# Kernel tuning notes

Hardware: AMD Instinct MI355X
Metric: run time of the kernel (lower is better)

The kernel has to match this reference:

```python
import jax, jax.numpy as jnp
import numpy as np

VOC_SIZE = 32768
DIM = 512
NUM_TOPK = 64
BATCH = 4096


def setup_inputs() -> dict:
    key = jax.random.key(0)
    ks = jax.random.split(key, 8)
    lim = 1.0 / np.sqrt(DIM)  # kaiming_uniform(a=sqrt(5)) on [V, d] -> U(-1/sqrt(d), 1/sqrt(d))
    x = jax.random.normal(ks[0], (BATCH, DIM), dtype=jnp.float32)
    codebook = jax.random.uniform(ks[1], (VOC_SIZE, DIM), dtype=jnp.float32, minval=-lim, maxval=lim)
    Wq = jax.random.uniform(ks[2], (DIM, DIM), dtype=jnp.float32, minval=-lim, maxval=lim)
    bq = jax.random.uniform(ks[3], (DIM,), dtype=jnp.float32, minval=-lim, maxval=lim)
    Wk = jax.random.uniform(ks[4], (DIM, DIM), dtype=jnp.float32, minval=-lim, maxval=lim)
    bk = jax.random.uniform(ks[5], (DIM,), dtype=jnp.float32, minval=-lim, maxval=lim)
    Wv = jax.random.uniform(ks[6], (DIM, DIM), dtype=jnp.float32, minval=-lim, maxval=lim)
    bv = jax.random.uniform(ks[7], (DIM,), dtype=jnp.float32, minval=-lim, maxval=lim)
    return {"x": x, "codebook": codebook, "Wq": Wq, "bq": bq,
            "Wk": Wk, "bk": bk, "Wv": Wv, "bv": bv}


def reference(x, codebook, Wq, bq, Wk, bk, Wv, bv):
    # projections (torch Linear with weight stored pre-transposed as [in, out])
    q = x @ Wq + bq              # [B, d]
    k = codebook @ Wk + bk       # [V, d]
    v = codebook @ Wv + bv       # [V, d]

    dots = jnp.einsum('bd,kd->bk', q, k)              # [B, V]
    top, _ = jax.lax.top_k(dots, NUM_TOPK)            # [B, num_topk]
    thresh = top[..., -1:]                            # k-th largest value per row
    mask_value = -jnp.finfo(dots.dtype).max
    dots = jnp.where(dots < thresh, mask_value, dots)
    attn = jax.nn.softmax(dots, axis=-1)              # [B, V]
    out = jnp.einsum('bk,kd->bd', attn, v)            # [B, d]
    return out
```

## Files before the change

kernel.cpp:

```cpp
#include <hip/hip_runtime.h>
#include <cstdint>

#define VOC   32768
#define DIM   512
#define TOPK  64
#define BATCH 4096

#define KSIG     2.45f
#define EPS_SEL  0.012f
#define CAND_CAP 512
#define RES_CAP  256
#define FCAP     1024

typedef unsigned short u16;
typedef __attribute__((ext_vector_type(8))) short bf16x8;
typedef __attribute__((ext_vector_type(4))) float f32x4;

__device__ __forceinline__ u16 f2bf(float f) {
    unsigned u = __float_as_uint(f);
    unsigned r = (u + 0x7FFFu + ((u >> 16) & 1u)) >> 16;
    return (u16)r;
}
__device__ __forceinline__ float bf2f(u16 h) {
    return __uint_as_float(((unsigned)h) << 16);
}
__device__ __forceinline__ unsigned enc16(u16 h) {
    return (h & 0x8000u) ? (unsigned)((u16)~h) : (unsigned)(h | 0x8000u);
}
__device__ __forceinline__ float dec16(unsigned s16) {
    u16 h = (s16 & 0x8000u) ? (u16)(s16 ^ 0x8000u) : (u16)(~s16);
    return bf2f(h);
}

__device__ __forceinline__ void async16(const void* g, void* l) {
    __builtin_amdgcn_global_load_lds(
        (const __attribute__((address_space(1))) void*)g,
        (__attribute__((address_space(3))) void*)l, 16, 0, 0);
}

template <bool BT, bool F64ACC>
__global__ __launch_bounds__(256)
void gemm64(const float* __restrict__ A, const float* __restrict__ B,
            const float* __restrict__ bias, float* __restrict__ C,
            int M, int N, int K)
{
    const int KS = 16;
    __shared__ float As[KS][68];
    __shared__ float Bs[KS][64];

    const int tid = threadIdx.x;
    const int m0 = blockIdx.y * 64;
    const int n0 = blockIdx.x * 64;
    const int ty = tid >> 4;
    const int tx = tid & 15;

    float acc[4][4];
    double acc64[4][4];
#pragma unroll
    for (int i = 0; i < 4; i++)
#pragma unroll
        for (int j = 0; j < 4; j++) { acc[i][j] = 0.f; if (F64ACC) acc64[i][j] = 0.0; }

    for (int kt = 0; kt < K; kt += KS) {
        {
            int row = tid >> 2, kq = tid & 3;
            const float4 av = *(const float4*)(A + (size_t)(m0 + row) * K + kt + kq * 4);
            As[kq * 4 + 0][row] = av.x;
            As[kq * 4 + 1][row] = av.y;
            As[kq * 4 + 2][row] = av.z;
            As[kq * 4 + 3][row] = av.w;
        }
        if (!BT) {
            int krow = tid >> 4, nq = tid & 15;
            *(float4*)&Bs[krow][nq * 4] =
                *(const float4*)(B + (size_t)(kt + krow) * N + n0 + nq * 4);
        } else {
            int nrow = tid >> 2, kq = tid & 3;
            const float4 bv = *(const float4*)(B + (size_t)(n0 + nrow) * K + kt + kq * 4);
            Bs[kq * 4 + 0][nrow] = bv.x;
            Bs[kq * 4 + 1][nrow] = bv.y;
            Bs[kq * 4 + 2][nrow] = bv.z;
            Bs[kq * 4 + 3][nrow] = bv.w;
        }
        __syncthreads();

#pragma unroll
        for (int kk = 0; kk < KS; kk++) {
            float4 a = *(const float4*)&As[kk][ty * 4];
            float4 b = *(const float4*)&Bs[kk][tx * 4];
            float av[4] = {a.x, a.y, a.z, a.w};
            float bv[4] = {b.x, b.y, b.z, b.w};
#pragma unroll
            for (int i = 0; i < 4; i++)
#pragma unroll
                for (int j = 0; j < 4; j++)
                    acc[i][j] += av[i] * bv[j];
        }
        __syncthreads();
        if (F64ACC) {
#pragma unroll
            for (int i = 0; i < 4; i++)
#pragma unroll
                for (int j = 0; j < 4; j++) { acc64[i][j] += (double)acc[i][j]; acc[i][j] = 0.f; }
        }
    }

    float4 bb = make_float4(0.f, 0.f, 0.f, 0.f);
    if (bias) bb = *(const float4*)(bias + n0 + tx * 4);
#pragma unroll
    for (int i = 0; i < 4; i++) {
        float4 o;
        o.x = (F64ACC ? (float)acc64[i][0] : acc[i][0]) + bb.x;
        o.y = (F64ACC ? (float)acc64[i][1] : acc[i][1]) + bb.y;
        o.z = (F64ACC ? (float)acc64[i][2] : acc[i][2]) + bb.z;
        o.w = (F64ACC ? (float)acc64[i][3] : acc[i][3]) + bb.w;
        *(float4*)(C + (size_t)(m0 + ty * 4 + i) * N + n0 + tx * 4) = o;
    }
}

__global__ void bias_fold(const float* __restrict__ bq, const float* __restrict__ Wk,
                          float* __restrict__ bqk)
{
    int j = blockIdx.x * 256 + threadIdx.x;
    if (j >= DIM) return;
    double s = 0.0;
    const float* wr = Wk + (size_t)j * DIM;
    for (int d = 0; d < DIM; d++) s += (double)bq[d] * (double)wr[d];
    bqk[j] = (float)s;
}

__global__ void zero_ws(unsigned* __restrict__ p, int n)
{
    int i = blockIdx.x * 256 + threadIdx.x;
    if (i < n) p[i] = 0u;
}

__global__ __launch_bounds__(256)
void cbar_accum(const float* __restrict__ cb, float* __restrict__ cbarsum)
{
    const int tid = threadIdx.x;
    const int r0 = blockIdx.x * 128;
    float s0 = 0.f, s1 = 0.f;
    for (int r = 0; r < 128; r++) {
        const float* rp = cb + (size_t)(r0 + r) * DIM;
        s0 += rp[tid];
        s1 += rp[tid + 256];
    }
    atomicAdd(&cbarsum[tid], s0);
    atomicAdd(&cbarsum[tid + 256], s1);
}

__global__ __launch_bounds__(256)
void rowstats(const float* __restrict__ q2, const float* __restrict__ cbarsum,
              float* __restrict__ trow, float* __restrict__ sigrow)
{
    const int tid = threadIdx.x, lane = tid & 63, wave = tid >> 6;
    const int row = blockIdx.x * 4 + wave;
    const float* qp = q2 + (size_t)row * DIM + lane * 8;
    float4 a0 = *(const float4*)qp, a1 = *(const float4*)(qp + 4);
    const float* cp = cbarsum + lane * 8;
    float4 c0 = *(const float4*)cp, c1 = *(const float4*)(cp + 4);
    float mu = a0.x*c0.x + a0.y*c0.y + a0.z*c0.z + a0.w*c0.w
             + a1.x*c1.x + a1.y*c1.y + a1.z*c1.z + a1.w*c1.w;
    float nr = a0.x*a0.x + a0.y*a0.y + a0.z*a0.z + a0.w*a0.w
             + a1.x*a1.x + a1.y*a1.y + a1.z*a1.z + a1.w*a1.w;
#pragma unroll
    for (int off = 32; off > 0; off >>= 1) {
        mu += __shfl_down(mu, off);
        nr += __shfl_down(nr, off);
    }
    if (lane == 0) {
        mu *= (1.f / VOC);
        float sig = sqrtf(nr * (1.f / 1536.f));
        trow[row] = mu + KSIG * sig;
        sigrow[row] = sig;
    }
}

__global__ __launch_bounds__(256)
void pack_rows(const float* __restrict__ src, u16* __restrict__ hi,
               u16* __restrict__ lo, int R, int log2R)
{
    int idx = blockIdx.x * 256 + threadIdx.x;
    int c8  = idx >> log2R;
    int row = idx & (R - 1);
    const float* sp = src + (size_t)row * DIM + c8 * 8;
    float xv[8];
    *(float4*)&xv[0] = *(const float4*)sp;
    *(float4*)&xv[4] = *(const float4*)(sp + 4);
    int ks = c8 >> 2, ch = c8 & 3;
    size_t ob = ((size_t)(ks * 4 + ch) * R + row) * 8;
    u16 h[8], l[8];
#pragma unroll
    for (int j = 0; j < 8; j++) {
        h[j] = f2bf(xv[j]);
        l[j] = f2bf(xv[j] - bf2f(h[j]));
    }
    *(uint4*)(hi + ob) = *(const uint4*)h;
    if (lo) *(uint4*)(lo + ob) = *(const uint4*)l;
}

__global__ __launch_bounds__(256)
void pack_bT(const float* __restrict__ W, u16* __restrict__ hi, u16* __restrict__ lo)
{
    int idx = blockIdx.x * 256 + threadIdx.x;
    int n  = idx & (DIM - 1);
    int c8 = idx >> 9;
    int ks = c8 >> 2, ch = c8 & 3;
    size_t ob = ((size_t)(ks * 4 + ch) * DIM + n) * 8;
    u16 h[8], l[8];
#pragma unroll
    for (int j = 0; j < 8; j++) {
        float x = W[(size_t)(c8 * 8 + j) * DIM + n];
        h[j] = f2bf(x);
        l[j] = f2bf(x - bf2f(h[j]));
    }
    *(uint4*)(hi + ob) = *(const uint4*)h;
    *(uint4*)(lo + ob) = *(const uint4*)l;
}

__global__ __launch_bounds__(256, 4)
void mfma_dots(const u16* __restrict__ Ah, const u16* __restrict__ Bh,
               const float* __restrict__ trow, unsigned* __restrict__ candBuf,
               unsigned* __restrict__ counters)
{
    __shared__ u16 lds[2 * 8192];

    const int tid  = threadIdx.x;
    const int lane = tid & 63;
    const int wave = tid >> 6;
    const int wm = wave >> 1, wn = wave & 1;
    const int lr = lane & 15;
    const int q  = lane >> 4;

    const int L   = blockIdx.x;
    const int xcd = L & 7;
    const int j   = L >> 3;
    const int m0  = (xcd * 4 + (j & 3)) * 128;
    const int n0  = (j >> 2) * 128;

    const int a  = wave >> 1;
    const u16* src = a ? Bh : Ah;
    const int rb   = a ? n0 : m0;
    const size_t R = a ? (size_t)VOC : (size_t)BATCH;
    const int i0   = (wave & 1) * 4;

    const size_t gstep = (size_t)4 * R * 8;
    const u16* gp0 = src + ((size_t)(((i0 + 0) >> 1)) * R + rb + ((i0 + 0) & 1) * 64 + lane) * 8;
    const u16* gp1 = src + ((size_t)(((i0 + 1) >> 1)) * R + rb + ((i0 + 1) & 1) * 64 + lane) * 8;
    const u16* gp2 = src + ((size_t)(((i0 + 2) >> 1)) * R + rb + ((i0 + 2) & 1) * 64 + lane) * 8;
    const u16* gp3 = src + ((size_t)(((i0 + 3) >> 1)) * R + rb + ((i0 + 3) & 1) * 64 + lane) * 8;
    const int loff0 = a * 4096 + (i0 + 0) * 512 + lane * 8;
    const int loff1 = a * 4096 + (i0 + 1) * 512 + lane * 8;
    const int loff2 = a * 4096 + (i0 + 2) * 512 + lane * 8;
    const int loff3 = a * 4096 + (i0 + 3) * 512 + lane * 8;

#define ISSUE(b)                                                              \
    {                                                                         \
        async16(gp0, &lds[(b) * 8192 + loff0]); gp0 += gstep;                 \
        async16(gp1, &lds[(b) * 8192 + loff1]); gp1 += gstep;                 \
        async16(gp2, &lds[(b) * 8192 + loff2]); gp2 += gstep;                 \
        async16(gp3, &lds[(b) * 8192 + loff3]); gp3 += gstep;                 \
    }

    f32x4 acc[4][4] = {};

    ISSUE(0)

    for (int s = 0; s < 16; s++) {
        __builtin_amdgcn_s_waitcnt(0x0F70);
        __builtin_amdgcn_s_barrier();
        if (s < 15) ISSUE((s + 1) & 1)
        const u16* base = &lds[(s & 1) * 8192];

        bf16x8 ah[4];
#pragma unroll
        for (int mt = 0; mt < 4; mt++)
            ah[mt] = *(const bf16x8*)&base[q * 1024 + (wm * 64 + mt * 16 + lr) * 8];
        __builtin_amdgcn_s_setprio(1);
#pragma unroll
        for (int nt = 0; nt < 4; nt++) {
            bf16x8 bh = *(const bf16x8*)&base[4096 + q * 1024 + (wn * 64 + nt * 16 + lr) * 8];
#pragma unroll
            for (int mt = 0; mt < 4; mt++)
                acc[mt][nt] = __builtin_amdgcn_mfma_f32_16x16x32_bf16(ah[mt], bh, acc[mt][nt], 0, 0, 0);
        }
        __builtin_amdgcn_s_setprio(0);
    }
#undef ISSUE

#pragma unroll
    for (int mt = 0; mt < 4; mt++) {
#pragma unroll
        for (int r = 0; r < 4; r++) {
            int rowg = m0 + wm * 64 + mt * 16 + q * 4 + r;
            float tr = trow[rowg];
#pragma unroll
            for (int nt = 0; nt < 4; nt++) {
                float val = acc[mt][nt][r];
                if (val >= tr) {
                    unsigned slot = atomicAdd(&counters[rowg], 1u);
                    if (slot < CAND_CAP) {
                        unsigned s16 = enc16(f2bf(val));
                        candBuf[(size_t)rowg * CAND_CAP + slot] =
                            (s16 << 16) | (unsigned)(n0 + wn * 64 + nt * 16 + lr);
                    }
                }
            }
        }
    }
}

__global__ __launch_bounds__(256, 2)
void mfma_out(const u16* __restrict__ Ah, const u16* __restrict__ Al,
              const u16* __restrict__ Bh, const u16* __restrict__ Bl,
              const float* __restrict__ bias, float* __restrict__ Cout, int Ma)
{
    __shared__ u16 lds[2 * 16384];

    const int tid  = threadIdx.x;
    const int lane = tid & 63;
    const int wave = tid >> 6;
    const int wm = wave >> 1, wn = wave & 1;
    const int m0 = blockIdx.y * 128, n0 = blockIdx.x * 128;
    const int lr = lane & 15;
    const int q  = lane >> 4;

    f32x4 acc[4][4] = {};
    const u16* garr[4] = {Ah, Bh, Al, Bl};
    const int a = wave;
    const u16* src = garr[a];
    const bool isA = (a == 0 || a == 2);
    const int rb = isA ? m0 : n0;
    const size_t R = isA ? (size_t)Ma : (size_t)DIM;

#define VISSUE(ks, b)                                                         \
    {                                                                         \
        _Pragma("unroll")                                                     \
        for (int i_ = 0; i_ < 8; i_++) {                                      \
            const u16* gp_ = src + ((size_t)((ks) * 4 + (i_ >> 1)) * R + rb   \
                                    + (i_ & 1) * 64 + lane) * 8;              \
            async16(gp_, &lds[(b) * 16384 + a * 4096 + i_ * 512 + lane * 8]); \
        }                                                                     \
    }

    VISSUE(0, 0)

    for (int ks = 0; ks < 16; ks++) {
        __syncthreads();
        if (ks < 15) VISSUE(ks + 1, (ks + 1) & 1)
        const u16* base = &lds[(ks & 1) * 16384];

        bf16x8 ah[4], al[4];
#pragma unroll
        for (int mt = 0; mt < 4; mt++) {
            int row = wm * 64 + mt * 16 + lr;
            ah[mt] = *(const bf16x8*)&base[0 * 4096 + q * 1024 + row * 8];
            al[mt] = *(const bf16x8*)&base[2 * 4096 + q * 1024 + row * 8];
        }
#pragma unroll
        for (int nt = 0; nt < 4; nt++) {
            int col = wn * 64 + nt * 16 + lr;
            bf16x8 bh = *(const bf16x8*)&base[1 * 4096 + q * 1024 + col * 8];
            bf16x8 bl = *(const bf16x8*)&base[3 * 4096 + q * 1024 + col * 8];
#pragma unroll
            for (int mt = 0; mt < 4; mt++) {
                acc[mt][nt] = __builtin_amdgcn_mfma_f32_16x16x32_bf16(ah[mt], bh, acc[mt][nt], 0, 0, 0);
                acc[mt][nt] = __builtin_amdgcn_mfma_f32_16x16x32_bf16(ah[mt], bl, acc[mt][nt], 0, 0, 0);
                acc[mt][nt] = __builtin_amdgcn_mfma_f32_16x16x32_bf16(al[mt], bh, acc[mt][nt], 0, 0, 0);
            }
        }
    }
#undef VISSUE

#pragma unroll
    for (int mt = 0; mt < 4; mt++)
#pragma unroll
        for (int nt = 0; nt < 4; nt++) {
            int col = n0 + wn * 64 + nt * 16 + lr;
            float bb = bias[col];
#pragma unroll
            for (int r = 0; r < 4; r++) {
                int rowg = m0 + wm * 64 + mt * 16 + q * 4 + r;
                Cout[(size_t)rowg * DIM + col] = acc[mt][nt][r] + bb;
            }
        }
}

__global__ __launch_bounds__(256)
void select6(const unsigned* __restrict__ candBuf, const unsigned* __restrict__ counters,
             const float* __restrict__ trow, const float* __restrict__ q2,
             const float* __restrict__ codebook, float* __restrict__ y,
             unsigned* __restrict__ flags)
{
    __shared__ unsigned recs[CAND_CAP];
    __shared__ unsigned list[RES_CAP];
    __shared__ unsigned hist[256];
    __shared__ unsigned long long keys[RES_CAP];
    __shared__ float q2s[DIM];
    __shared__ float wArr[RES_CAP];
    __shared__ float redf[256];
    __shared__ unsigned redu[256];
    __shared__ unsigned s_R;
    __shared__ unsigned s_b1, s_rem, s_thr;

    const int tid  = threadIdx.x;
    const int lane = tid & 63;
    const int wave = tid >> 6;
    const int row  = blockIdx.x;

    const unsigned cnt = counters[row];
    if (cnt < TOPK || cnt > CAND_CAP) {
        if (tid == 0) flags[row] = 1u;
        return;
    }
    for (int i = tid; i < DIM; i += 256) q2s[i] = q2[(size_t)row * DIM + i];
    for (int i = tid; i < CAND_CAP; i += 256)
        recs[i] = (i < (int)cnt) ? candBuf[(size_t)row * CAND_CAP + i] : 0u;
    if (tid == 0) s_R = 0;
    hist[tid] = 0;
    __syncthreads();

#pragma unroll
    for (int e = 0; e < 2; e++) {
        int i = tid + e * 256;
        if (i < (int)cnt) atomicAdd(&hist[recs[i] >> 24], 1u);
    }
    __syncthreads();
    if (tid == 0) {
        unsigned c = 0; int b = 255;
        for (; b > 0; b--) {
            unsigned h = hist[b];
            if (c + h >= TOPK) break;
            c += h;
        }
        s_b1 = (unsigned)b; s_rem = TOPK - c;
    }
    __syncthreads();
    const unsigned b1 = s_b1, rem = s_rem;
    hist[tid] = 0;
    __syncthreads();

#pragma unroll
    for (int e = 0; e < 2; e++) {
        int i = tid + e * 256;
        if (i < (int)cnt && (recs[i] >> 24) == b1)
            atomicAdd(&hist[(recs[i] >> 16) & 0xFFu], 1u);
    }
    __syncthreads();
    if (tid == 0) {
        unsigned c = 0; int b = 255;
        for (; b > 0; b--) {
            unsigned h = hist[b];
            if (c + h >= rem) break;
            c += h;
        }
        s_thr = (b1 << 8) | (unsigned)b;
    }
    __syncthreads();

    const float a64  = dec16(s_thr);
    const float band = a64 - 2.f * EPS_SEL;
    if (trow[row] > band) {
        if (tid == 0) flags[row] = 1u;
        return;
    }

#pragma unroll
    for (int e = 0; e < 2; e++) {
        int i = tid + e * 256;
        if (i < (int)cnt && dec16(recs[i] >> 16) >= band) {
            unsigned p = atomicAdd(&s_R, 1u);
            if (p < RES_CAP) list[p] = recs[i];
        }
    }
    __syncthreads();
    const int R = (int)s_R;
    if (R > RES_CAP) {
        if (tid == 0) flags[row] = 1u;
        return;
    }

    for (int c = wave; c < R; c += 4) {
        unsigned idx = list[c] & 0xFFFFu;
        const float* cb = codebook + (size_t)idx * DIM + lane * 8;
        float4 c0 = *(const float4*)cb, c1 = *(const float4*)(cb + 4);
        const float* qp = &q2s[lane * 8];
        float4 a0 = *(const float4*)qp, a1 = *(const float4*)(qp + 4);
        double s = (double)a0.x * c0.x + (double)a0.y * c0.y
                 + (double)a0.z * c0.z + (double)a0.w * c0.w
                 + (double)a1.x * c1.x + (double)a1.y * c1.y
                 + (double)a1.z * c1.z + (double)a1.w * c1.w;
#pragma unroll
        for (int off = 32; off > 0; off >>= 1) s += __shfl_down(s, off);
        if (lane == 0) {
            float val = (float)s;
            unsigned b = __float_as_uint(val);
            unsigned sk = (b & 0x80000000u) ? ~b : (b | 0x80000000u);
            keys[c] = ((unsigned long long)(~sk) << 32) | idx;
        }
    }
    if (tid >= R && tid < RES_CAP) keys[tid] = ~0ULL;
    __syncthreads();

    for (int k = 2; k <= RES_CAP; k <<= 1) {
        for (int j = k >> 1; j > 0; j >>= 1) {
            int ixj = tid ^ j;
            if (ixj > tid) {
                unsigned long long a = keys[tid], b2 = keys[ixj];
                if (((tid & k) == 0) ? (a > b2) : (a < b2)) { keys[tid] = b2; keys[ixj] = a; }
            }
            __syncthreads();
        }
    }

    const unsigned threshInv = (unsigned)(keys[TOPK - 1] >> 32);
    unsigned sk0 = ~(unsigned)(keys[0] >> 32);
    const float vmax = __uint_as_float((sk0 & 0x80000000u) ? (sk0 & 0x7FFFFFFFu) : ~sk0);

    unsigned hi = (unsigned)(keys[tid] >> 32);
    bool sel = (hi <= threshInv);
    unsigned sk = ~hi;
    float val = __uint_as_float((sk & 0x80000000u) ? (sk & 0x7FFFFFFFu) : ~sk);
    float w = sel ? expf(val - vmax) : 0.f;
    wArr[tid] = w;
    redf[tid] = w;
    redu[tid] = sel ? 1u : 0u;
    __syncthreads();
    for (int s = 128; s > 0; s >>= 1) {
        if (tid < s) { redf[tid] += redf[tid + s]; redu[tid] += redu[tid + s]; }
        __syncthreads();
    }
    const float invZ = 1.0f / redf[0];
    const int selCount = (int)redu[0];

    for (int d = tid; d < DIM; d += 256) {
        float acc = 0.f;
        for (int i = 0; i < selCount; i++) {
            unsigned idx = (unsigned)(keys[i] & 0xFFFFFFFFu);
            acc += wArr[i] * codebook[(size_t)idx * DIM + d];
        }
        y[(size_t)row * DIM + d] = acc * invZ;
    }
}

__global__ __launch_bounds__(256)
void fallback_row(const unsigned* __restrict__ flags, const float* __restrict__ q2,
                  const float* __restrict__ codebook, const float* __restrict__ trow,
                  const float* __restrict__ sigrow, float* __restrict__ y)
{
    const int row = blockIdx.x;
    if (!flags[row]) return;

    __shared__ float q2s[DIM];
    __shared__ unsigned long long keys[FCAP];
    __shared__ float wArr[FCAP];
    __shared__ float redf[256];
    __shared__ unsigned redu[256];
    __shared__ unsigned s_cnt;

    const int tid = threadIdx.x;
    for (int i = tid; i < DIM; i += 256) q2s[i] = q2[(size_t)row * DIM + i];
    const float sig = sigrow[row];
    float tf = trow[row] - 0.35f * sig;
    unsigned cnt = 0;

    for (int it = 0; it < 16; it++) {
        if (tid == 0) s_cnt = 0;
        __syncthreads();
        for (int i = tid; i < VOC; i += 256) {
            const float* cb = codebook + (size_t)i * DIM;
            double s = 0.0;
            for (int d = 0; d < DIM; d += 4) {
                float4 c4 = *(const float4*)(cb + d);
                s += (double)q2s[d + 0] * (double)c4.x + (double)q2s[d + 1] * (double)c4.y
                   + (double)q2s[d + 2] * (double)c4.z + (double)q2s[d + 3] * (double)c4.w;
            }
            float vv = (float)s;
            if (vv >= tf) {
                unsigned p = atomicAdd(&s_cnt, 1u);
                if (p < FCAP) {
                    unsigned b = __float_as_uint(vv);
                    unsigned sk = (b & 0x80000000u) ? ~b : (b | 0x80000000u);
                    keys[p] = ((unsigned long long)(~sk) << 32) | (unsigned)i;
                }
            }
        }
        __syncthreads();
        cnt = s_cnt;
        if (cnt > FCAP) { tf += 0.15f * sig; continue; }
        if (cnt < TOPK) { tf -= 0.35f * sig; continue; }
        break;
    }
    if (cnt > FCAP) cnt = FCAP;
    for (int i = tid; i < FCAP; i += 256)
        if (i >= (int)cnt) keys[i] = ~0ULL;
    __syncthreads();

    for (int k = 2; k <= FCAP; k <<= 1) {
        for (int j = k >> 1; j > 0; j >>= 1) {
#pragma unroll
            for (int e = 0; e < 4; e++) {
                int i = tid + e * 256;
                int ixj = i ^ j;
                if (ixj > i) {
                    unsigned long long a = keys[i], b = keys[ixj];
                    if (((i & k) == 0) ? (a > b) : (a < b)) { keys[i] = b; keys[ixj] = a; }
                }
            }
            __syncthreads();
        }
    }

    const unsigned threshInv = (unsigned)(keys[TOPK - 1] >> 32);
    unsigned sk0 = ~(unsigned)(keys[0] >> 32);
    const float vmax = __uint_as_float((sk0 & 0x80000000u) ? (sk0 & 0x7FFFFFFFu) : ~sk0);

    float lsum = 0.f; unsigned lcnt = 0;
    for (int i = tid; i < FCAP; i += 256) {
        unsigned hi = (unsigned)(keys[i] >> 32);
        bool sel = (hi <= threshInv);
        unsigned sk = ~hi;
        float vv = __uint_as_float((sk & 0x80000000u) ? (sk & 0x7FFFFFFFu) : ~sk);
        float w = sel ? expf(vv - vmax) : 0.f;
        wArr[i] = w;
        lsum += w; lcnt += sel ? 1u : 0u;
    }
    redf[tid] = lsum; redu[tid] = lcnt;
    __syncthreads();
    for (int s = 128; s > 0; s >>= 1) {
        if (tid < s) { redf[tid] += redf[tid + s]; redu[tid] += redu[tid + s]; }
        __syncthreads();
    }
    const float invZ = 1.f / redf[0];
    const int selCount = (int)redu[0];

    for (int d = tid; d < DIM; d += 256) {
        float acc = 0.f;
        for (int i = 0; i < selCount; i++) {
            unsigned idx = (unsigned)(keys[i] & 0xFFFFFFFFu);
            acc += wArr[i] * codebook[(size_t)idx * DIM + d];
        }
        y[(size_t)row * DIM + d] = acc * invZ;
    }
}

extern "C" void kernel_launch(void* const* d_in, const int* in_sizes, int n_in,
                              void* d_out, int out_size, void* d_ws, size_t ws_size,
                              hipStream_t stream)
{
    const float* x        = (const float*)d_in[0];
    const float* codebook = (const float*)d_in[1];
    const float* Wq       = (const float*)d_in[2];
    const float* bq       = (const float*)d_in[3];
    const float* Wk       = (const float*)d_in[4];
    const float* Wv       = (const float*)d_in[6];
    const float* bv       = (const float*)d_in[7];
    float* out = (float*)d_out;

    float* q2   = (float*)d_ws;
    float* Wqk  = q2   + (size_t)BATCH * DIM;
    float* bqk  = Wqk  + (size_t)DIM * DIM;
    float* y    = bqk  + 1024;
    float* trow = y    + (size_t)BATCH * DIM;
    float* sigr = trow + BATCH;
    unsigned* counters = (unsigned*)(sigr + BATCH);
    unsigned* flags    = counters + BATCH;
    float* cbarsum     = (float*)(flags + BATCH);
    unsigned* candBuf  = (unsigned*)(cbarsum + 512);
    u16* q2h = (u16*)(candBuf + (size_t)BATCH * CAND_CAP);
    u16* cbh = q2h + (size_t)BATCH * DIM;
    u16* yh  = cbh + (size_t)VOC * DIM;
    u16* yl  = yh  + (size_t)BATCH * DIM;
    u16* wvh = yl  + (size_t)BATCH * DIM;
    u16* wvl = wvh + (size_t)DIM * DIM;

    u16* xh   = yh;
    u16* xl   = yl;
    u16* wqkh = (u16*)candBuf;
    u16* wqkl = wqkh + (size_t)DIM * DIM;

    dim3 blk(256);

    gemm64<true, true><<<dim3(DIM / 64, DIM / 64), blk, 0, stream>>>(
        Wq, Wk, nullptr, Wqk, DIM, DIM, DIM);
    bias_fold<<<dim3(2), blk, 0, stream>>>(bq, Wk, bqk);

    pack_bT<<<dim3(DIM * 64 / 256), blk, 0, stream>>>(Wqk, wqkh, wqkl);
    pack_rows<<<dim3(BATCH * 64 / 256), blk, 0, stream>>>(x, xh, xl, BATCH, 12);
    mfma_out<<<dim3(DIM / 128, BATCH / 128), blk, 0, stream>>>(
        xh, xl, wqkh, wqkl, bqk, q2, BATCH);

    zero_ws<<<dim3(34), blk, 0, stream>>>(counters, BATCH * 2 + 512);

    cbar_accum<<<dim3(VOC / 128), blk, 0, stream>>>(codebook, cbarsum);
    rowstats<<<dim3(BATCH / 4), blk, 0, stream>>>(q2, cbarsum, trow, sigr);

    pack_rows<<<dim3(BATCH * 64 / 256), blk, 0, stream>>>(q2, q2h, nullptr, BATCH, 12);
    pack_rows<<<dim3(VOC * 64 / 256), blk, 0, stream>>>(codebook, cbh, nullptr, VOC, 15);
    pack_bT<<<dim3(DIM * 64 / 256), blk, 0, stream>>>(Wv, wvh, wvl);

    mfma_dots<<<dim3(8192), blk, 0, stream>>>(q2h, cbh, trow, candBuf, counters);

    select6<<<dim3(BATCH), blk, 0, stream>>>(
        candBuf, counters, trow, q2, codebook, y, flags);
    fallback_row<<<dim3(BATCH), blk, 0, stream>>>(
        flags, q2, codebook, trow, sigr, y);

    pack_rows<<<dim3(BATCH * 64 / 256), blk, 0, stream>>>(y, yh, yl, BATCH, 12);
    mfma_out<<<dim3(DIM / 128, BATCH / 128), blk, 0, stream>>>(
        yh, yl, wvh, wvl, bv, out, BATCH);
}
```

Before: 678.9 us.

## Load B fragments directly to registers in mfma_dots and parallelize bias_fold

After: 689.7 us. About the same (+1.6%).

```diff
diff --git a/kernel.cpp b/kernel.cpp
--- a/kernel.cpp
+++ b/kernel.cpp
@@ -118,15 +118,20 @@
     }
 }
 
-__global__ void bias_fold(const float* __restrict__ bq, const float* __restrict__ Wk,
-                          float* __restrict__ bqk)
-{
-    int j = blockIdx.x * 256 + threadIdx.x;
-    if (j >= DIM) return;
+__global__ __launch_bounds__(256)
+void bias_fold(const float* __restrict__ bq, const float* __restrict__ Wk,
+               float* __restrict__ bqk)
+{
+    const int lane = threadIdx.x & 63, wave = threadIdx.x >> 6;
+    const int j = blockIdx.x * 4 + wave;
+    const float* wr = Wk + (size_t)j * DIM + lane * 8;
+    const float* bp = bq + lane * 8;
     double s = 0.0;
-    const float* wr = Wk + (size_t)j * DIM;
-    for (int d = 0; d < DIM; d++) s += (double)bq[d] * (double)wr[d];
-    bqk[j] = (float)s;
+#pragma unroll
+    for (int t = 0; t < 8; t++) s += (double)bp[t] * (double)wr[t];
+#pragma unroll
+    for (int off = 32; off > 0; off >>= 1) s += __shfl_down(s, off);
+    if (lane == 0) bqk[j] = (float)s;
 }
 
 __global__ void zero_ws(unsigned* __restrict__ p, int n)
@@ -224,7 +229,7 @@
                const float* __restrict__ trow, unsigned* __restrict__ candBuf,
                unsigned* __restrict__ counters)
 {
-    __shared__ u16 lds[2 * 8192];
+    __shared__ u16 lds[4 * 4096];
 
     const int tid  = threadIdx.x;
     const int lane = tid & 63;
@@ -239,55 +244,53 @@
     const int m0  = (xcd * 4 + (j & 3)) * 128;
     const int n0  = (j >> 2) * 128;
 
-    const int a  = wave >> 1;
-    const u16* src = a ? Bh : Ah;
-    const int rb   = a ? n0 : m0;
-    const size_t R = a ? (size_t)VOC : (size_t)BATCH;
-    const int i0   = (wave & 1) * 4;
-
-    const size_t gstep = (size_t)4 * R * 8;
-    const u16* gp0 = src + ((size_t)(((i0 + 0) >> 1)) * R + rb + ((i0 + 0) & 1) * 64 + lane) * 8;
-    const u16* gp1 = src + ((size_t)(((i0 + 1) >> 1)) * R + rb + ((i0 + 1) & 1) * 64 + lane) * 8;
-    const u16* gp2 = src + ((size_t)(((i0 + 2) >> 1)) * R + rb + ((i0 + 2) & 1) * 64 + lane) * 8;
-    const u16* gp3 = src + ((size_t)(((i0 + 3) >> 1)) * R + rb + ((i0 + 3) & 1) * 64 + lane) * 8;
-    const int loff0 = a * 4096 + (i0 + 0) * 512 + lane * 8;
-    const int loff1 = a * 4096 + (i0 + 1) * 512 + lane * 8;
-    const int loff2 = a * 4096 + (i0 + 2) * 512 + lane * 8;
-    const int loff3 = a * 4096 + (i0 + 3) * 512 + lane * 8;
-
-#define ISSUE(b)                                                              \
-    {                                                                         \
-        async16(gp0, &lds[(b) * 8192 + loff0]); gp0 += gstep;                 \
-        async16(gp1, &lds[(b) * 8192 + loff1]); gp1 += gstep;                 \
-        async16(gp2, &lds[(b) * 8192 + loff2]); gp2 += gstep;                 \
-        async16(gp3, &lds[(b) * 8192 + loff3]); gp3 += gstep;                 \
-    }
+    u16* wlds = &lds[wave * 4096];
+
+#define AISSUE(ks, st)                                                         \
+    { _Pragma("unroll")                                                        \
+      for (int ch_ = 0; ch_ < 4; ch_++) {                                      \
+          const u16* gp_ = Ah + ((size_t)((ks) * 4 + ch_) * BATCH              \
+                                 + m0 + wm * 64 + lane) * 8;                   \
+          async16(gp_, &wlds[(st) * 2048 + ch_ * 512 + lane * 8]);             \
+      } }
+
+#define BPTR(nt, ks) ((const bf16x8*)(Bh + ((size_t)((ks) * 4 + q) * VOC       \
+                                            + n0 + wn * 64 + (nt) * 16 + lr) * 8))
 
     f32x4 acc[4][4] = {};
-
-    ISSUE(0)
-
+    bf16x8 bb[2][4];
+
+    AISSUE(0, 0)
+#pragma unroll
+    for (int nt = 0; nt < 4; nt++) bb[0][nt] = *BPTR(nt, 0);
+
+#pragma unroll
     for (int s = 0; s < 16; s++) {
+        const int st = s & 1;
         __builtin_amdgcn_s_waitcnt(0x0F70);
-        __builtin_amdgcn_s_barrier();
-        if (s < 15) ISSUE((s + 1) & 1)
-        const u16* base = &lds[(s & 1) * 8192];
 
         bf16x8 ah[4];
 #pragma unroll
         for (int mt = 0; mt < 4; mt++)
-            ah[mt] = *(const bf16x8*)&base[q * 1024 + (wm * 64 + mt * 16 + lr) * 8];
+            ah[mt] = *(const bf16x8*)&wlds[st * 2048 + q * 512 + (mt * 16 + lr) * 8];
+
+        __builtin_amdgcn_sched_barrier(0);
+        __builtin_amdgcn_s_waitcnt(0xC47F);
+        if (s < 15) AISSUE(s + 1, st ^ 1)
+
         __builtin_amdgcn_s_setprio(1);
 #pragma unroll
         for (int nt = 0; nt < 4; nt++) {
-            bf16x8 bh = *(const bf16x8*)&base[4096 + q * 1024 + (wn * 64 + nt * 16 + lr) * 8];
+            if (s < 15) bb[st ^ 1][nt] = *BPTR(nt, s + 1);
 #pragma unroll
             for (int mt = 0; mt < 4; mt++)
-                acc[mt][nt] = __builtin_amdgcn_mfma_f32_16x16x32_bf16(ah[mt], bh, acc[mt][nt], 0, 0, 0);
+                acc[mt][nt] = __builtin_amdgcn_mfma_f32_16x16x32_bf16(
+                    ah[mt], bb[st][nt], acc[mt][nt], 0, 0, 0);
         }
         __builtin_amdgcn_s_setprio(0);
     }
-#undef ISSUE
+#undef AISSUE
+#undef BPTR
 
 #pragma unroll
     for (int mt = 0; mt < 4; mt++) {
@@ -684,7 +687,7 @@
 
     gemm64<true, true><<<dim3(DIM / 64, DIM / 64), blk, 0, stream>>>(
         Wq, Wk, nullptr, Wqk, DIM, DIM, DIM);
-    bias_fold<<<dim3(2), blk, 0, stream>>>(bq, Wk, bqk);
+    bias_fold<<<dim3(DIM / 4), blk, 0, stream>>>(bq, Wk, bqk);
 
     pack_bT<<<dim3(DIM * 64 / 256), blk, 0, stream>>>(Wqk, wqkh, wqkl);
     pack_rows<<<dim3(BATCH * 64 / 256), blk, 0, stream>>>(x, xh, xl, BATCH, 12);
```

## Fuse prep kernels into two launches and restructure dots loop prefetch

Applied to the files above, without the earlier changes.

Result: faster. 643.0 us (-5.3%).

```diff
diff --git a/kernel.cpp b/kernel.cpp
--- a/kernel.cpp
+++ b/kernel.cpp
@@ -118,70 +118,17 @@
     }
 }
 
-__global__ void bias_fold(const float* __restrict__ bq, const float* __restrict__ Wk,
-                          float* __restrict__ bqk)
-{
-    int j = blockIdx.x * 256 + threadIdx.x;
-    if (j >= DIM) return;
-    double s = 0.0;
-    const float* wr = Wk + (size_t)j * DIM;
-    for (int d = 0; d < DIM; d++) s += (double)bq[d] * (double)wr[d];
-    bqk[j] = (float)s;
-}
-
 __global__ void zero_ws(unsigned* __restrict__ p, int n)
 {
     int i = blockIdx.x * 256 + threadIdx.x;
     if (i < n) p[i] = 0u;
 }
 
-__global__ __launch_bounds__(256)
-void cbar_accum(const float* __restrict__ cb, float* __restrict__ cbarsum)
-{
-    const int tid = threadIdx.x;
-    const int r0 = blockIdx.x * 128;
-    float s0 = 0.f, s1 = 0.f;
-    for (int r = 0; r < 128; r++) {
-        const float* rp = cb + (size_t)(r0 + r) * DIM;
-        s0 += rp[tid];
-        s1 += rp[tid + 256];
-    }
-    atomicAdd(&cbarsum[tid], s0);
-    atomicAdd(&cbarsum[tid + 256], s1);
-}
-
-__global__ __launch_bounds__(256)
-void rowstats(const float* __restrict__ q2, const float* __restrict__ cbarsum,
-              float* __restrict__ trow, float* __restrict__ sigrow)
-{
-    const int tid = threadIdx.x, lane = tid & 63, wave = tid >> 6;
-    const int row = blockIdx.x * 4 + wave;
-    const float* qp = q2 + (size_t)row * DIM + lane * 8;
-    float4 a0 = *(const float4*)qp, a1 = *(const float4*)(qp + 4);
-    const float* cp = cbarsum + lane * 8;
-    float4 c0 = *(const float4*)cp, c1 = *(const float4*)(cp + 4);
-    float mu = a0.x*c0.x + a0.y*c0.y + a0.z*c0.z + a0.w*c0.w
-             + a1.x*c1.x + a1.y*c1.y + a1.z*c1.z + a1.w*c1.w;
-    float nr = a0.x*a0.x + a0.y*a0.y + a0.z*a0.z + a0.w*a0.w
-             + a1.x*a1.x + a1.y*a1.y + a1.z*a1.z + a1.w*a1.w;
-#pragma unroll
-    for (int off = 32; off > 0; off >>= 1) {
-        mu += __shfl_down(mu, off);
-        nr += __shfl_down(nr, off);
-    }
-    if (lane == 0) {
-        mu *= (1.f / VOC);
-        float sig = sqrtf(nr * (1.f / 1536.f));
-        trow[row] = mu + KSIG * sig;
-        sigrow[row] = sig;
-    }
-}
-
-__global__ __launch_bounds__(256)
-void pack_rows(const float* __restrict__ src, u16* __restrict__ hi,
-               u16* __restrict__ lo, int R, int log2R)
-{
-    int idx = blockIdx.x * 256 + threadIdx.x;
+__device__ __forceinline__ void pack_rows_dev(int bid, int tid,
+        const float* __restrict__ src, u16* __restrict__ hi,
+        u16* __restrict__ lo, int R, int log2R)
+{
+    int idx = bid * 256 + tid;
     int c8  = idx >> log2R;
     int row = idx & (R - 1);
     const float* sp = src + (size_t)row * DIM + c8 * 8;
@@ -200,10 +147,10 @@
     if (lo) *(uint4*)(lo + ob) = *(const uint4*)l;
 }
 
-__global__ __launch_bounds__(256)
-void pack_bT(const float* __restrict__ W, u16* __restrict__ hi, u16* __restrict__ lo)
-{
-    int idx = blockIdx.x * 256 + threadIdx.x;
+__device__ __forceinline__ void pack_bT_dev(int bid, int tid,
+        const float* __restrict__ W, u16* __restrict__ hi, u16* __restrict__ lo)
+{
+    int idx = bid * 256 + tid;
     int n  = idx & (DIM - 1);
     int c8 = idx >> 9;
     int ks = c8 >> 2, ch = c8 & 3;
@@ -217,6 +164,99 @@
     }
     *(uint4*)(hi + ob) = *(const uint4*)h;
     *(uint4*)(lo + ob) = *(const uint4*)l;
+}
+
+__device__ __forceinline__ void cbar_dev(int bid, int tid,
+        const float* __restrict__ cb, float* __restrict__ cbarsum)
+{
+    const int r0 = bid * 128;
+    float s0 = 0.f, s1 = 0.f;
+    for (int r = 0; r < 128; r++) {
+        const float* rp = cb + (size_t)(r0 + r) * DIM;
+        s0 += rp[tid];
+        s1 += rp[tid + 256];
+    }
+    atomicAdd(&cbarsum[tid], s0);
+    atomicAdd(&cbarsum[tid + 256], s1);
+}
+
+__device__ __forceinline__ void bias_fold_dev(int bid, int tid,
+        const float* __restrict__ bq, const float* __restrict__ Wk,
+        float* __restrict__ bqk)
+{
+    const int lane = tid & 63, wave = tid >> 6;
+    const int j = bid * 4 + wave;
+    const float* wr = Wk + (size_t)j * DIM + lane * 8;
+    const float* bp = bq + lane * 8;
+    double s = 0.0;
+#pragma unroll
+    for (int t = 0; t < 8; t++) s += (double)bp[t] * (double)wr[t];
+#pragma unroll
+    for (int off = 32; off > 0; off >>= 1) s += __shfl_down(s, off);
+    if (lane == 0) bqk[j] = (float)s;
+}
+
+__device__ __forceinline__ void rowstats_dev(int bid, int tid,
+        const float* __restrict__ q2, const float* __restrict__ cbarsum,
+        float* __restrict__ trow, float* __restrict__ sigrow)
+{
+    const int lane = tid & 63, wave = tid >> 6;
+    const int row = bid * 4 + wave;
+    const float* qp = q2 + (size_t)row * DIM + lane * 8;
+    float4 a0 = *(const float4*)qp, a1 = *(const float4*)(qp + 4);
+    const float* cp = cbarsum + lane * 8;
+    float4 c0 = *(const float4*)cp, c1 = *(const float4*)(cp + 4);
+    float mu = a0.x*c0.x + a0.y*c0.y + a0.z*c0.z + a0.w*c0.w
+             + a1.x*c1.x + a1.y*c1.y + a1.z*c1.z + a1.w*c1.w;
+    float nr = a0.x*a0.x + a0.y*a0.y + a0.z*a0.z + a0.w*a0.w
+             + a1.x*a1.x + a1.y*a1.y + a1.z*a1.z + a1.w*a1.w;
+#pragma unroll
+    for (int off = 32; off > 0; off >>= 1) {
+        mu += __shfl_down(mu, off);
+        nr += __shfl_down(nr, off);
+    }
+    if (lane == 0) {
+        mu *= (1.f / VOC);
+        float sig = sqrtf(nr * (1.f / 1536.f));
+        trow[row] = mu + KSIG * sig;
+        sigrow[row] = sig;
+    }
+}
+
+__global__ __launch_bounds__(256)
+void fused_prep(const float* __restrict__ x, const float* __restrict__ Wqk,
+                const float* __restrict__ codebook, const float* __restrict__ Wv,
+                const float* __restrict__ bq, const float* __restrict__ Wk,
+                u16* __restrict__ xh, u16* __restrict__ xl,
+                u16* __restrict__ wqkh, u16* __restrict__ wqkl,
+                u16* __restrict__ cbh, u16* __restrict__ wvh,
+                u16* __restrict__ wvl, float* __restrict__ cbarsum,
+                float* __restrict__ bqk)
+{
+    const int b = blockIdx.x, tid = threadIdx.x;
+    if (b < 1024)       pack_rows_dev(b, tid, x, xh, xl, BATCH, 12);
+    else if (b < 1152)  pack_bT_dev(b - 1024, tid, Wqk, wqkh, wqkl);
+    else if (b < 9344)  pack_rows_dev(b - 1152, tid, codebook, cbh, nullptr, VOC, 15);
+    else if (b < 9472)  pack_bT_dev(b - 9344, tid, Wv, wvh, wvl);
+    else if (b < 9728)  cbar_dev(b - 9472, tid, codebook, cbarsum);
+    else                bias_fold_dev(b - 9728, tid, bq, Wk, bqk);
+}
+
+__global__ __launch_bounds__(256)
+void fused_q2post(const float* __restrict__ q2, const float* __restrict__ cbarsum,
+                  float* __restrict__ trow, float* __restrict__ sigrow,
+                  u16* __restrict__ q2h)
+{
+    const int b = blockIdx.x, tid = threadIdx.x;
+    if (b < 1024) rowstats_dev(b, tid, q2, cbarsum, trow, sigrow);
+    else          pack_rows_dev(b - 1024, tid, q2, q2h, nullptr, BATCH, 12);
+}
+
+__global__ __launch_bounds__(256)
+void pack_rows(const float* __restrict__ src, u16* __restrict__ hi,
+               u16* __restrict__ lo, int R, int log2R)
+{
+    pack_rows_dev(blockIdx.x, threadIdx.x, src, hi, lo, R, log2R);
 }
 
 __global__ __launch_bounds__(256, 4)
@@ -266,25 +306,39 @@
     f32x4 acc[4][4] = {};
 
     ISSUE(0)
+    ISSUE(1)
 
     for (int s = 0; s < 16; s++) {
-        __builtin_amdgcn_s_waitcnt(0x0F70);
+        if (s < 15) __builtin_amdgcn_s_waitcnt(0x0F74);
+        else        __builtin_amdgcn_s_waitcnt(0x0F70);
         __builtin_amdgcn_s_barrier();
-        if (s < 15) ISSUE((s + 1) & 1)
         const u16* base = &lds[(s & 1) * 8192];
 
         bf16x8 ah[4];
 #pragma unroll
         for (int mt = 0; mt < 4; mt++)
             ah[mt] = *(const bf16x8*)&base[q * 1024 + (wm * 64 + mt * 16 + lr) * 8];
+
         __builtin_amdgcn_s_setprio(1);
 #pragma unroll
-        for (int nt = 0; nt < 4; nt++) {
+        for (int nt = 0; nt < 3; nt++) {
             bf16x8 bh = *(const bf16x8*)&base[4096 + q * 1024 + (wn * 64 + nt * 16 + lr) * 8];
 #pragma unroll
             for (int mt = 0; mt < 4; mt++)
                 acc[mt][nt] = __builtin_amdgcn_mfma_f32_16x16x32_bf16(ah[mt], bh, acc[mt][nt], 0, 0, 0);
         }
+        bf16x8 bh3 = *(const bf16x8*)&base[4096 + q * 1024 + (wn * 64 + 3 * 16 + lr) * 8];
+        __builtin_amdgcn_s_setprio(0);
+
+        __builtin_amdgcn_s_waitcnt(0xC07F);
+        __builtin_amdgcn_s_barrier();
+        __builtin_amdgcn_sched_barrier(0);
+        if (s < 14) ISSUE(s & 1)
+
+        __builtin_amdgcn_s_setprio(1);
+#pragma unroll
+        for (int mt = 0; mt < 4; mt++)
+            acc[mt][3] = __builtin_amdgcn_mfma_f32_16x16x32_bf16(ah[mt], bh3, acc[mt][3], 0, 0, 0);
         __builtin_amdgcn_s_setprio(0);
     }
 #undef ISSUE
@@ -682,23 +736,19 @@
 
     dim3 blk(256);
 
+    zero_ws<<<dim3(34), blk, 0, stream>>>(counters, BATCH * 2 + 512);
+
     gemm64<true, true><<<dim3(DIM / 64, DIM / 64), blk, 0, stream>>>(
         Wq, Wk, nullptr, Wqk, DIM, DIM, DIM);
-    bias_fold<<<dim3(2), blk, 0, stream>>>(bq, Wk, bqk);
-
-    pack_bT<<<dim3(DIM * 64 / 256), blk, 0, stream>>>(Wqk, wqkh, wqkl);
-    pack_rows<<<dim3(BATCH * 64 / 256), blk, 0, stream>>>(x, xh, xl, BATCH, 12);
+
+    fused_prep<<<dim3(9856), blk, 0, stream>>>(
+        x, Wqk, codebook, Wv, bq, Wk,
+        xh, xl, wqkh, wqkl, cbh, wvh, wvl, cbarsum, bqk);
+
     mfma_out<<<dim3(DIM / 128, BATCH / 128), blk, 0, stream>>>(
         xh, xl, wqkh, wqkl, bqk, q2, BATCH);
 
-    zero_ws<<<dim3(34), blk, 0, stream>>>(counters, BATCH * 2 + 512);
-
-    cbar_accum<<<dim3(VOC / 128), blk, 0, stream>>>(codebook, cbarsum);
-    rowstats<<<dim3(BATCH / 4), blk, 0, stream>>>(q2, cbarsum, trow, sigr);
-
-    pack_rows<<<dim3(BATCH * 64 / 256), blk, 0, stream>>>(q2, q2h, nullptr, BATCH, 12);
-    pack_rows<<<dim3(VOC * 64 / 256), blk, 0, stream>>>(codebook, cbh, nullptr, VOC, 15);
-    pack_bT<<<dim3(DIM * 64 / 256), blk, 0, stream>>>(Wv, wvh, wvl);
+    fused_q2post<<<dim3(2048), blk, 0, stream>>>(q2, cbarsum, trow, sigr, q2h);
 
     mfma_dots<<<dim3(8192), blk, 0, stream>>>(q2h, cbh, trow, candBuf, counters);
 
```
